# Kernel optimization log

Measured on AMD Instinct MI355X. Metric: run time of the kernel, lower is better.

## Reference

```python
import jax, jax.numpy as jnp
import numpy as np

B, N, M, C1, C2 = 16, 4096, 1024, 128, 256
MLP0, MLP1 = 256, 256
IN_CH = C1 + C2
EPS = 1e-5


def setup_inputs() -> dict:
    key = jax.random.key(0)
    ks = jax.random.split(key, 6)
    return {
        "xyz1": jax.random.normal(ks[0], (B, 3, N), jnp.float32),
        "xyz2": jax.random.normal(ks[1], (B, 3, M), jnp.float32),
        "points1": jax.random.normal(ks[2], (B, C1, N), jnp.float32),
        "points2": jax.random.normal(ks[3], (B, C2, M), jnp.float32),
        "W1": jax.random.normal(ks[4], (MLP0, IN_CH), jnp.float32) * (1.0 / np.sqrt(IN_CH)),
        "gamma1": jnp.ones((MLP0,), jnp.float32),
        "beta1": jnp.zeros((MLP0,), jnp.float32),
        "W2": jax.random.normal(ks[5], (MLP1, MLP0), jnp.float32) * (1.0 / np.sqrt(MLP0)),
        "gamma2": jnp.ones((MLP1,), jnp.float32),
        "beta2": jnp.zeros((MLP1,), jnp.float32),
    }


def _batchnorm(x, gamma, beta):
    # x: (B, N, C); normalize per channel over batch*length (training-mode BN, biased var)
    mean = jnp.mean(x, axis=(0, 1))
    var = jnp.mean((x - mean) ** 2, axis=(0, 1))
    return (x - mean) * jax.lax.rsqrt(var + EPS) * gamma + beta


def reference(xyz1, xyz2, points1, points2, W1, gamma1, beta1, W2, gamma2, beta2):
    p1 = jnp.swapaxes(xyz1, 1, 2)  # (B, N, 3)
    p2 = jnp.swapaxes(xyz2, 1, 2)  # (B, M, 3)
    # squared pairwise distances (B, N, M); squaring preserves 3-NN ordering,
    # and the original squares the euclidean dist before weighting anyway
    d2 = jnp.sum((p1[:, :, None, :] - p2[:, None, :, :]) ** 2, axis=-1)
    neg_d2, idx = jax.lax.top_k(-d2, 3)  # 3 smallest distances
    dist2 = jnp.maximum(-neg_d2, 1e-10)  # (B, N, 3)
    inv = 1.0 / dist2
    weight = inv / jnp.sum(inv, axis=-1, keepdims=True)  # (B, N, 3)
    f2 = jnp.swapaxes(points2, 1, 2)  # (B, M, C2)
    b, n, k = idx.shape
    gathered = jnp.take_along_axis(
        f2, idx.reshape(b, n * k)[:, :, None], axis=1
    ).reshape(b, n, k, -1)  # (B, N, 3, C2)
    interp = jnp.einsum("bnk,bnkc->bnc", weight, gathered)  # (B, N, C2)
    feat = jnp.concatenate([interp, jnp.swapaxes(points1, 1, 2)], axis=-1)  # (B, N, C1+C2)
    h = jnp.einsum("bnc,oc->bno", feat, W1)  # conv1d k=1, no bias
    h = jax.nn.relu(_batchnorm(h, gamma1, beta1))
    h = jnp.einsum("bnc,oc->bno", h, W2)
    h = jax.nn.relu(_batchnorm(h, gamma2, beta2))
    return jnp.swapaxes(h, 1, 2)  # (B, MLP1, N), channel-first like torch
```

## Files before the change

### kernel.cpp

```cpp
#include <hip/hip_runtime.h>

typedef unsigned short u16;
typedef unsigned int u32;

#define BB 16
#define NN 4096
#define MM 1024
#define C1V 128
#define C2V 256
#define O1 256
#define O2 256
#define EPSV 1e-5f
#define INV_CNT (1.0f/65536.0f)
#define NREP 32

typedef __attribute__((ext_vector_type(8))) short bf16x8;
typedef __attribute__((ext_vector_type(4))) float f32x4;

static __device__ __forceinline__ u16 f2b(float f) {
  u32 u = __float_as_uint(f);
  u32 r = (u + 0x7FFFu + ((u >> 16) & 1u)) >> 16;
  return (u16)r;
}
static __device__ __forceinline__ float b2f(u16 s) {
  return __uint_as_float(((u32)s) << 16);
}

#define GLD_LDS16(gp, lp)                                                      \
  __builtin_amdgcn_global_load_lds(                                            \
      (const __attribute__((address_space(1))) void*)(gp),                     \
      (__attribute__((address_space(3))) void*)(lp), 16, 0, 0)

__device__ __forceinline__ void tcast_tile(const float* __restrict__ in,
                                           u16* __restrict__ out, int C, int P,
                                           int p0, int c0, int b,
                                           float (*tile)[33]) {
  int tx = threadIdx.x & 31, ty = threadIdx.x >> 5;
  const float* ib = in + (size_t)b * C * P;
  u16* ob = out + (size_t)b * P * C;
#pragma unroll
  for (int i = 0; i < 4; ++i)
    tile[ty + i * 8][tx] = ib[(size_t)(c0 + ty + i * 8) * P + p0 + tx];
  __syncthreads();
#pragma unroll
  for (int i = 0; i < 4; ++i)
    ob[(size_t)(p0 + ty + i * 8) * C + c0 + tx] = f2b(tile[tx][ty + i * 8]);
}

__global__ __launch_bounds__(256) void prep_kernel(
    const float* __restrict__ xyz1, const float* __restrict__ xyz2,
    float* __restrict__ pd, int* __restrict__ pi,
    const float* __restrict__ points1, const float* __restrict__ points2,
    u16* __restrict__ p1t, u16* __restrict__ p2t,
    const float* __restrict__ W1, const float* __restrict__ W2,
    u16* __restrict__ W1b, u16* __restrict__ W2b,
    float* __restrict__ statsZero) {
  __shared__ float4 cand[256];
  __shared__ float tile[32][33];
  int bx = blockIdx.x;
  int t = threadIdx.x;

  if (bx < 512) {
    int c = bx & 3;
    int qt = (bx >> 2) & 7;
    int b = bx >> 5;
    const float* x2b = xyz2 + b * 3 * MM;
    {
      float x = x2b[c * 256 + t];
      float y = x2b[MM + c * 256 + t];
      float z = x2b[2 * MM + c * 256 + t];
      cand[t] = make_float4(x, y, z, x * x + y * y + z * z);
    }
    __syncthreads();
    const float* x1b = xyz1 + b * 3 * NN;
    int n0 = qt * 512 + t;
    int n1 = n0 + 256;
    float px0 = x1b[n0], py0 = x1b[NN + n0], pz0 = x1b[2 * NN + n0];
    float px1 = x1b[n1], py1 = x1b[NN + n1], pz1 = x1b[2 * NN + n1];
    const float INF = 3.4e38f;
    float k00 = INF, k01 = INF, k02 = INF;
    float k10 = INF, k11 = INF, k12 = INF;
    int j00 = 0, j01 = 0, j02 = 0;
    int j10 = 0, j11 = 0, j12 = 0;
#pragma unroll 8
    for (int m = 0; m < 256; ++m) {
      float4 cd = cand[m];
      {
        float dot = fmaf(px0, cd.x, fmaf(py0, cd.y, pz0 * cd.z));
        float key = fmaf(-2.0f, dot, cd.w);
        bool c0 = key < k00, c1 = key < k01, c2 = key < k02;
        k02 = c1 ? k01 : (c2 ? key : k02);
        j02 = c1 ? j01 : (c2 ? m : j02);
        k01 = c0 ? k00 : (c1 ? key : k01);
        j01 = c0 ? j00 : (c1 ? m : j01);
        k00 = c0 ? key : k00;
        j00 = c0 ? m : j00;
      }
      {
        float dot = fmaf(px1, cd.x, fmaf(py1, cd.y, pz1 * cd.z));
        float key = fmaf(-2.0f, dot, cd.w);
        bool c0 = key < k10, c1 = key < k11, c2 = key < k12;
        k12 = c1 ? k11 : (c2 ? key : k12);
        j12 = c1 ? j11 : (c2 ? m : j12);
        k11 = c0 ? k10 : (c1 ? key : k11);
        j11 = c0 ? j10 : (c1 ? m : j11);
        k10 = c0 ? key : k10;
        j10 = c0 ? m : j10;
      }
    }
    float pn0 = px0 * px0 + py0 * py0 + pz0 * pz0;
    float pn1 = px1 * px1 + py1 * py1 + pz1 * pz1;
    int gq0 = b * NN + n0;
    int gq1 = b * NN + n1;
    int base = c << 8;
    ((float4*)pd)[(size_t)c * 65536 + gq0] =
        make_float4(fmaxf(k00 + pn0, 1e-10f), fmaxf(k01 + pn0, 1e-10f),
                    fmaxf(k02 + pn0, 1e-10f), 0.0f);
    ((int4*)pi)[(size_t)c * 65536 + gq0] =
        make_int4(base + j00, base + j01, base + j02, 0);
    ((float4*)pd)[(size_t)c * 65536 + gq1] =
        make_float4(fmaxf(k10 + pn1, 1e-10f), fmaxf(k11 + pn1, 1e-10f),
                    fmaxf(k12 + pn1, 1e-10f), 0.0f);
    ((int4*)pi)[(size_t)c * 65536 + gq1] =
        make_int4(base + j10, base + j11, base + j12, 0);
  } else if (bx < 1152) {
    int i = (bx - 512) * 256 + t;
    if (i < 98304) W1b[i] = f2b(W1[i]);
    else if (i < 163840) W2b[i - 98304] = f2b(W2[i - 98304]);
  } else if (bx < 1184) {
    ((float4*)statsZero)[(bx - 1152) * 256 + t] =
        make_float4(0.f, 0.f, 0.f, 0.f);
  } else if (bx < 5280) {
    int local = bx - 1184;
    int pt = local & 31, ct = (local >> 5) & 7, b = local >> 8;
    tcast_tile(points2, p2t, C2V, MM, pt * 32, ct * 32, b, tile);
  } else {
    int local = bx - 5280;
    int pt = local & 127, ct = (local >> 7) & 3, b = local >> 9;
    tcast_tile(points1, p1t, C1V, NN, pt * 32, ct * 32, b, tile);
  }
}

template <int K, int NTILES, bool INTERP, bool STATS, bool OUTB, bool BNA>
__global__ __launch_bounds__(256) void gemm_mfma(
    const u16* __restrict__ A, int lda, const u16* __restrict__ B, int ldb,
    void* __restrict__ out, const u16* __restrict__ G,
    const float* __restrict__ pd, const int* __restrict__ pi,
    float* __restrict__ statsOut, const float* __restrict__ statsInR,
    const float* __restrict__ gamma, const float* __restrict__ beta) {
  __shared__ u16 smem[16384];
  __shared__ float wsh[128][3];
  __shared__ int ish[128][3];
  __shared__ float scA[256], shA[256];

  int t = threadIdx.x;
  int w = t >> 6, l = t & 63;
  int n0;
  if (NTILES > 0) {
    int p = blockIdx.x;
    int batch = ((p & 7) << 1) | ((p >> 3) & 1);
    int nt = p >> 4;
    n0 = (batch * NTILES + nt) * 128;
  } else {
    n0 = blockIdx.x * 128;
  }
  int o0 = blockIdx.y * 128;

  if (INTERP) {
    if (t < 128) {
      int gq = n0 + t;
      float4 d0 = ((const float4*)pd)[gq];
      int4 ii0 = ((const int4*)pi)[gq];
      float a0 = d0.x, a1 = d0.y, a2 = d0.z;
      int b0 = ii0.x, b1 = ii0.y, b2 = ii0.z;
#pragma unroll
      for (int c = 1; c < 4; ++c) {
        float4 dc = ((const float4*)pd)[(size_t)c * 65536 + gq];
        int4 ic = ((const int4*)pi)[(size_t)c * 65536 + gq];
        float kv[3] = {dc.x, dc.y, dc.z};
        int jv[3] = {ic.x, ic.y, ic.z};
#pragma unroll
        for (int j = 0; j < 3; ++j) {
          float key = kv[j];
          int idx = jv[j];
          bool c0 = key < a0, c1 = key < a1, c2 = key < a2;
          a2 = c1 ? a1 : (c2 ? key : a2);
          b2 = c1 ? b1 : (c2 ? idx : b2);
          a1 = c0 ? a0 : (c1 ? key : a1);
          b1 = c0 ? b0 : (c1 ? idx : b1);
          a0 = c0 ? key : a0;
          b0 = c0 ? idx : b0;
        }
      }
      float v0 = 1.0f / a0, v1 = 1.0f / a1, v2 = 1.0f / a2;
      float s = 1.0f / (v0 + v1 + v2);
      wsh[t][0] = v0 * s; wsh[t][1] = v1 * s; wsh[t][2] = v2 * s;
      ish[t][0] = b0;     ish[t][1] = b1;     ish[t][2] = b2;
    }
  }
  if (BNA) {
    float s = 0.0f, qq = 0.0f;
#pragma unroll
    for (int r = 0; r < NREP; ++r) {
      s += statsInR[r * 512 + t];
      qq += statsInR[r * 512 + 256 + t];
    }
    float mean = s * INV_CNT;
    float var = qq * INV_CNT - mean * mean;
    float sc = rsqrtf(var + EPSV) * gamma[t];
    scA[t] = sc;
    shA[t] = beta[t] - mean * sc;
  }

  int wm = w & 1, wn = w >> 1;
  int lr = l >> 2, lc = l & 3;
  int q = l >> 4, m = l & 15;

  f32x4 acc[4][4] = {};
  u16* As = smem;
  u16* Bs = smem + 4096;

  const u16* arow = A + (size_t)n0 * lda;
  const u16* brow = B + (size_t)o0 * ldb;

#pragma unroll
  for (int kt = 0; kt < K; kt += 32) {
    __syncthreads();
#pragma unroll
    for (int r = 0; r < 2; ++r) {
      int row = r * 64 + w * 16 + lr;
      if (BNA) {
        union { uint4 u; u16 s[8]; } v, o;
        v.u = *(const uint4*)(arow + (size_t)row * lda + kt + lc * 8);
        int cb = kt + lc * 8;
#pragma unroll
        for (int j = 0; j < 8; ++j) {
          float f = fmaf(b2f(v.s[j]), scA[cb + j], shA[cb + j]);
          o.s[j] = f2b(fmaxf(f, 0.0f));
        }
        *(uint4*)(As + row * 32 + lc * 8) = o.u;
      } else {
        GLD_LDS16(arow + (size_t)row * lda + kt + lc * 8, As + row * 32 + lc * 8);
      }
    }
#pragma unroll
    for (int r = 0; r < 2; ++r) {
      int row = r * 64 + w * 16 + lr;
      GLD_LDS16(brow + (size_t)row * ldb + kt + lc * 8, Bs + row * 32 + lc * 8);
    }
    __syncthreads();
    bf16x8 af[4], bf[4];
#pragma unroll
    for (int i = 0; i < 4; ++i)
      af[i] = *(const bf16x8*)(As + (wm * 64 + i * 16 + m) * 32 + q * 8);
#pragma unroll
    for (int j = 0; j < 4; ++j)
      bf[j] = *(const bf16x8*)(Bs + (wn * 64 + j * 16 + m) * 32 + q * 8);
#pragma unroll
    for (int i = 0; i < 4; ++i)
#pragma unroll
      for (int j = 0; j < 4; ++j)
        acc[i][j] =
            __builtin_amdgcn_mfma_f32_16x16x32_bf16(af[i], bf[j], acc[i][j], 0, 0, 0);
  }

  if (INTERP) {
    __syncthreads();
    int b = n0 >> 12;
    int rl = t >> 1, half = t & 1, rx = rl & 7;
    float w0 = wsh[rl][0], w1 = wsh[rl][1], w2 = wsh[rl][2];
    const u16* g0 = G + ((size_t)(b * 1024 + ish[rl][0])) * 256 + o0 + half * 64;
    const u16* g1 = G + ((size_t)(b * 1024 + ish[rl][1])) * 256 + o0 + half * 64;
    const u16* g2 = G + ((size_t)(b * 1024 + ish[rl][2])) * 256 + o0 + half * 64;
#pragma unroll
    for (int c8 = 0; c8 < 8; ++c8) {
      bf16x8 v0 = *(const bf16x8*)(g0 + c8 * 8);
      bf16x8 v1 = *(const bf16x8*)(g1 + c8 * 8);
      bf16x8 v2 = *(const bf16x8*)(g2 + c8 * 8);
      union { uint4 u; u16 s[8]; } o;
#pragma unroll
      for (int e = 0; e < 8; ++e) {
        float f = w0 * b2f((u16)v0[e]) + w1 * b2f((u16)v1[e]) +
                  w2 * b2f((u16)v2[e]);
        o.s[e] = f2b(f);
      }
      int ch = (half * 8 + c8) ^ rx;
      *(uint4*)(smem + rl * 128 + ch * 8) = o.u;
    }
    __syncthreads();
#pragma unroll
    for (int i = 0; i < 4; ++i)
#pragma unroll
      for (int reg = 0; reg < 4; ++reg) {
        int row = wm * 64 + i * 16 + q * 4 + reg;
        int rxr = row & 7;
#pragma unroll
        for (int j = 0; j < 4; ++j) {
          int col = wn * 64 + j * 16 + m;
          int off = row * 128 + (((col >> 3) ^ rxr) << 3) + (col & 7);
          acc[i][j][reg] += b2f(smem[off]);
        }
      }
  }

  if (STATS) {
    int rep = blockIdx.x & (NREP - 1);
#pragma unroll
    for (int j = 0; j < 4; ++j) {
      float s = 0.0f, ss = 0.0f;
#pragma unroll
      for (int i = 0; i < 4; ++i)
#pragma unroll
        for (int reg = 0; reg < 4; ++reg) {
          float v = acc[i][j][reg];
          s += v;
          ss += v * v;
        }
      s += __shfl_down(s, 32); ss += __shfl_down(ss, 32);
      s += __shfl_down(s, 16); ss += __shfl_down(ss, 16);
      if (l < 16) {
        int c = o0 + wn * 64 + j * 16 + l;
        atomicAdd(&statsOut[rep * 512 + c], s);
        atomicAdd(&statsOut[rep * 512 + 256 + c], ss);
      }
    }
  }

  if (OUTB) {
    __syncthreads();
#pragma unroll
    for (int i = 0; i < 4; ++i)
#pragma unroll
      for (int reg = 0; reg < 4; ++reg) {
        int row = wm * 64 + i * 16 + q * 4 + reg;
#pragma unroll
        for (int j = 0; j < 4; ++j)
          smem[row * 128 + wn * 64 + j * 16 + m] = f2b(acc[i][j][reg]);
      }
    __syncthreads();
    u16* outp = (u16*)out;
    int rbase = w * 32 + (l >> 4);
    int seg = l & 15;
#pragma unroll
    for (int itr = 0; itr < 8; ++itr) {
      int row = rbase + itr * 4;
      uint4 v = *(const uint4*)(smem + row * 128 + seg * 8);
      *(uint4*)(outp + (size_t)(n0 + row) * 256 + o0 + seg * 8) = v;
    }
  } else {
#pragma unroll
    for (int i = 0; i < 4; ++i) {
      int gr = n0 + wm * 64 + i * 16 + q * 4;
#pragma unroll
      for (int reg = 0; reg < 4; ++reg)
#pragma unroll
        for (int j = 0; j < 4; ++j) {
          int gc = o0 + wn * 64 + j * 16 + m;
          ((float*)out)[(size_t)(gr + reg) * 256 + gc] = acc[i][j][reg];
        }
    }
  }
}

__global__ __launch_bounds__(256) void bn2t_kernel(
    const u16* __restrict__ h2, const float* __restrict__ statsR,
    const float* __restrict__ gamma, const float* __restrict__ beta,
    float* __restrict__ out) {
  __shared__ float tile[32][33];
  __shared__ float sS[32], sH[32];
  int t = threadIdx.x;
  int tx = t & 31, ty = t >> 5;
  int n0 = blockIdx.x * 32, c0 = blockIdx.y * 32, b = blockIdx.z;
  if (t < 32) {
    int c = c0 + t;
    float s = 0.0f, qq = 0.0f;
#pragma unroll
    for (int r = 0; r < NREP; ++r) {
      s += statsR[r * 512 + c];
      qq += statsR[r * 512 + 256 + c];
    }
    float mean = s * INV_CNT;
    float var = qq * INV_CNT - mean * mean;
    float sc = rsqrtf(var + EPSV) * gamma[c];
    sS[t] = sc;
    sH[t] = beta[c] - mean * sc;
  }
  __syncthreads();
#pragma unroll
  for (int i = 0; i < 4; ++i) {
    int n = n0 + ty + i * 8;
    float v = b2f(h2[((size_t)b * NN + n) * 256 + c0 + tx]) * sS[tx] + sH[tx];
    tile[ty + i * 8][tx] = fmaxf(v, 0.0f);
  }
  __syncthreads();
#pragma unroll
  for (int i = 0; i < 4; ++i)
    out[((size_t)b * 256 + c0 + ty + i * 8) * NN + n0 + tx] = tile[tx][ty + i * 8];
}

extern "C" void kernel_launch(void* const* d_in, const int* in_sizes, int n_in,
                              void* d_out, int out_size, void* d_ws,
                              size_t ws_size, hipStream_t stream) {
  const float* xyz1    = (const float*)d_in[0];
  const float* xyz2    = (const float*)d_in[1];
  const float* points1 = (const float*)d_in[2];
  const float* points2 = (const float*)d_in[3];
  const float* W1      = (const float*)d_in[4];
  const float* gamma1  = (const float*)d_in[5];
  const float* beta1   = (const float*)d_in[6];
  const float* W2      = (const float*)d_in[7];
  const float* gamma2  = (const float*)d_in[8];
  const float* beta2   = (const float*)d_in[9];

  char* ws = (char*)d_ws;
  float* stats1R = (float*)(ws + 0);
  float* stats2R = (float*)(ws + 65536);
  u16*   W1b     = (u16*)(ws + 131072);
  u16*   W2b     = (u16*)(ws + 327680);
  u16*   p2t     = (u16*)(ws + 458752);
  u16*   p1t     = (u16*)(ws + 8847360);
  u16*   G       = (u16*)(ws + 25624576);
  u16*   h2b     = (u16*)(ws + 34013184);
  float* pd      = (float*)(ws + 67567616);
  int*   pi      = (int*)(ws + 71761920);
  u16*   h1b     = (u16*)d_out;
  float* out     = (float*)d_out;

  prep_kernel<<<13472, 256, 0, stream>>>(xyz1, xyz2, pd, pi, points1, points2,
                                         p1t, p2t, W1, W2, W1b, W2b, stats1R);
  gemm_mfma<256, 8, false, false, true, false><<<dim3(128, 2), 256, 0, stream>>>(
      p2t, 256, W1b, 384, G, nullptr, nullptr, nullptr, nullptr, nullptr,
      nullptr, nullptr);
  gemm_mfma<128, 32, true, true, true, false><<<dim3(512, 2), 256, 0, stream>>>(
      p1t, 128, W1b + 256, 384, h1b, G, pd, pi, stats1R, nullptr, nullptr,
      nullptr);
  gemm_mfma<256, 0, false, true, true, true><<<dim3(512, 2), 256, 0, stream>>>(
      h1b, 256, W2b, 256, h2b, nullptr, nullptr, nullptr, stats2R, stats1R,
      gamma1, beta1);
  bn2t_kernel<<<dim3(128, 8, 16), 256, 0, stream>>>(h2b, stats2R, gamma2,
                                                    beta2, out);
}
```

Measured before the change: 232.5 us.

## Fuse BN2+ReLU+transpose into second GEMM via grid-wide barrier

```diff
diff --git a/kernel.cpp b/kernel.cpp
--- a/kernel.cpp
+++ b/kernel.cpp
@@ -8,8 +8,6 @@
 #define MM 1024
 #define C1V 128
 #define C2V 256
-#define O1 256
-#define O2 256
 #define EPSV 1e-5f
 #define INV_CNT (1.0f/65536.0f)
 #define NREP 32
@@ -54,7 +52,7 @@
     u16* __restrict__ p1t, u16* __restrict__ p2t,
     const float* __restrict__ W1, const float* __restrict__ W2,
     u16* __restrict__ W1b, u16* __restrict__ W2b,
-    float* __restrict__ statsZero) {
+    float* __restrict__ statsZero, int* __restrict__ bar) {
   __shared__ float4 cand[256];
   __shared__ float tile[32][33];
   int bx = blockIdx.x;
@@ -130,6 +128,7 @@
   } else if (bx < 1184) {
     ((float4*)statsZero)[(bx - 1152) * 256 + t] =
         make_float4(0.f, 0.f, 0.f, 0.f);
+    if (bx == 1152 && t == 0) *bar = 0;
   } else if (bx < 5280) {
     int local = bx - 1184;
     int pt = local & 31, ct = (local >> 5) & 7, b = local >> 8;
@@ -141,17 +140,21 @@
   }
 }
 
-template <int K, int NTILES, bool INTERP, bool STATS, bool OUTB, bool BNA>
-__global__ __launch_bounds__(256) void gemm_mfma(
+template <int K, int NTILES, int NJ, bool INTERP, bool STATS, bool OUTB,
+          bool BNA, bool FUSE>
+__global__ __launch_bounds__(256, 2) void gemm_mfma(
     const u16* __restrict__ A, int lda, const u16* __restrict__ B, int ldb,
     void* __restrict__ out, const u16* __restrict__ G,
     const float* __restrict__ pd, const int* __restrict__ pi,
     float* __restrict__ statsOut, const float* __restrict__ statsInR,
-    const float* __restrict__ gamma, const float* __restrict__ beta) {
-  __shared__ u16 smem[16384];
+    const float* __restrict__ gamma, const float* __restrict__ beta,
+    const float* __restrict__ gamma2, const float* __restrict__ beta2,
+    int* bar, float* __restrict__ fout) {
+  __shared__ __align__(16) u16 smem[NJ == 8 ? 16896 : 16384];
   __shared__ float wsh[128][3];
   __shared__ int ish[128][3];
   __shared__ float scA[256], shA[256];
+  __shared__ float scB[256], shB[256];
 
   int t = threadIdx.x;
   int w = t >> 6, l = t & 63;
@@ -164,7 +167,7 @@
   } else {
     n0 = blockIdx.x * 128;
   }
-  int o0 = blockIdx.y * 128;
+  int o0 = blockIdx.y * (NJ * 32);
 
   if (INTERP) {
     if (t < 128) {
@@ -216,7 +219,7 @@
   int lr = l >> 2, lc = l & 3;
   int q = l >> 4, m = l & 15;
 
-  f32x4 acc[4][4] = {};
+  f32x4 acc[4][NJ] = {};
   u16* As = smem;
   u16* Bs = smem + 4096;
 
@@ -244,22 +247,22 @@
       }
     }
 #pragma unroll
-    for (int r = 0; r < 2; ++r) {
+    for (int r = 0; r < NJ / 2; ++r) {
       int row = r * 64 + w * 16 + lr;
       GLD_LDS16(brow + (size_t)row * ldb + kt + lc * 8, Bs + row * 32 + lc * 8);
     }
     __syncthreads();
-    bf16x8 af[4], bf[4];
+    bf16x8 af[4], bf[NJ];
 #pragma unroll
     for (int i = 0; i < 4; ++i)
       af[i] = *(const bf16x8*)(As + (wm * 64 + i * 16 + m) * 32 + q * 8);
 #pragma unroll
-    for (int j = 0; j < 4; ++j)
-      bf[j] = *(const bf16x8*)(Bs + (wn * 64 + j * 16 + m) * 32 + q * 8);
+    for (int j = 0; j < NJ; ++j)
+      bf[j] = *(const bf16x8*)(Bs + (wn * (NJ * 16) + j * 16 + m) * 32 + q * 8);
 #pragma unroll
     for (int i = 0; i < 4; ++i)
 #pragma unroll
-      for (int j = 0; j < 4; ++j)
+      for (int j = 0; j < NJ; ++j)
         acc[i][j] =
             __builtin_amdgcn_mfma_f32_16x16x32_bf16(af[i], bf[j], acc[i][j], 0, 0, 0);
   }
@@ -295,8 +298,8 @@
         int row = wm * 64 + i * 16 + q * 4 + reg;
         int rxr = row & 7;
 #pragma unroll
-        for (int j = 0; j < 4; ++j) {
-          int col = wn * 64 + j * 16 + m;
+        for (int j = 0; j < NJ; ++j) {
+          int col = wn * (NJ * 16) + j * 16 + m;
           int off = row * 128 + (((col >> 3) ^ rxr) << 3) + (col & 7);
           acc[i][j][reg] += b2f(smem[off]);
         }
@@ -306,7 +309,7 @@
   if (STATS) {
     int rep = blockIdx.x & (NREP - 1);
 #pragma unroll
-    for (int j = 0; j < 4; ++j) {
+    for (int j = 0; j < NJ; ++j) {
       float s = 0.0f, ss = 0.0f;
 #pragma unroll
       for (int i = 0; i < 4; ++i)
@@ -319,7 +322,7 @@
       s += __shfl_down(s, 32); ss += __shfl_down(ss, 32);
       s += __shfl_down(s, 16); ss += __shfl_down(ss, 16);
       if (l < 16) {
-        int c = o0 + wn * 64 + j * 16 + l;
+        int c = o0 + wn * (NJ * 16) + j * 16 + l;
         atomicAdd(&statsOut[rep * 512 + c], s);
         atomicAdd(&statsOut[rep * 512 + 256 + c], ss);
       }
@@ -334,8 +337,8 @@
       for (int reg = 0; reg < 4; ++reg) {
         int row = wm * 64 + i * 16 + q * 4 + reg;
 #pragma unroll
-        for (int j = 0; j < 4; ++j)
-          smem[row * 128 + wn * 64 + j * 16 + m] = f2b(acc[i][j][reg]);
+        for (int j = 0; j < NJ; ++j)
+          smem[row * 128 + wn * (NJ * 16) + j * 16 + m] = f2b(acc[i][j][reg]);
       }
     __syncthreads();
     u16* outp = (u16*)out;
@@ -347,6 +350,63 @@
       uint4 v = *(const uint4*)(smem + row * 128 + seg * 8);
       *(uint4*)(outp + (size_t)(n0 + row) * 256 + o0 + seg * 8) = v;
     }
+  } else if (FUSE) {
+    __syncthreads();
+    if (t == 0) {
+      __hip_atomic_fetch_add(bar, 1, __ATOMIC_ACQ_REL, __HIP_MEMORY_SCOPE_AGENT);
+      while (__hip_atomic_load(bar, __ATOMIC_ACQUIRE, __HIP_MEMORY_SCOPE_AGENT) <
+             (int)gridDim.x)
+        __builtin_amdgcn_s_sleep(8);
+    }
+    __syncthreads();
+    {
+      float s = 0.0f, qq = 0.0f;
+#pragma unroll
+      for (int r = 0; r < NREP; ++r) {
+        s += __hip_atomic_load(&statsOut[r * 512 + t], __ATOMIC_RELAXED,
+                               __HIP_MEMORY_SCOPE_AGENT);
+        qq += __hip_atomic_load(&statsOut[r * 512 + 256 + t], __ATOMIC_RELAXED,
+                                __HIP_MEMORY_SCOPE_AGENT);
+      }
+      float mean = s * INV_CNT;
+      float var = qq * INV_CNT - mean * mean;
+      float sc = rsqrtf(var + EPSV) * gamma2[t];
+      scB[t] = sc;
+      shB[t] = beta2[t] - mean * sc;
+    }
+    __syncthreads();
+    int b = n0 >> 12, nin = n0 & 4095;
+#pragma unroll
+    for (int h = 0; h < 2; ++h) {
+      if (h) __syncthreads();
+      if (wn == h) {
+#pragma unroll
+        for (int i = 0; i < 4; ++i)
+#pragma unroll
+          for (int j = 0; j < NJ; ++j) {
+            int c = j * 16 + m;
+            float sc = scB[h * 128 + c], sh = shB[h * 128 + c];
+#pragma unroll
+            for (int reg = 0; reg < 4; ++reg) {
+              int row = wm * 64 + i * 16 + q * 4 + reg;
+              smem[c * 132 + row] =
+                  f2b(fmaxf(fmaf(acc[i][j][reg], sc, sh), 0.0f));
+            }
+          }
+      }
+      __syncthreads();
+      int hl = l >> 5, nl = (l & 31) * 4;
+#pragma unroll
+      for (int it = 0; it < 16; ++it) {
+        int cl = w * 32 + it * 2 + hl;
+        uint2 vv = *(const uint2*)(smem + cl * 132 + nl);
+        float4 o4 = make_float4(
+            b2f((u16)(vv.x & 0xffff)), b2f((u16)(vv.x >> 16)),
+            b2f((u16)(vv.y & 0xffff)), b2f((u16)(vv.y >> 16)));
+        *(float4*)(fout + ((size_t)(b * 256 + h * 128 + cl)) * 4096 + nin + nl) =
+            o4;
+      }
+    }
   } else {
 #pragma unroll
     for (int i = 0; i < 4; ++i) {
@@ -354,48 +414,12 @@
 #pragma unroll
       for (int reg = 0; reg < 4; ++reg)
 #pragma unroll
-        for (int j = 0; j < 4; ++j) {
-          int gc = o0 + wn * 64 + j * 16 + m;
+        for (int j = 0; j < NJ; ++j) {
+          int gc = o0 + wn * (NJ * 16) + j * 16 + m;
           ((float*)out)[(size_t)(gr + reg) * 256 + gc] = acc[i][j][reg];
         }
     }
   }
-}
-
-__global__ __launch_bounds__(256) void bn2t_kernel(
-    const u16* __restrict__ h2, const float* __restrict__ statsR,
-    const float* __restrict__ gamma, const float* __restrict__ beta,
-    float* __restrict__ out) {
-  __shared__ float tile[32][33];
-  __shared__ float sS[32], sH[32];
-  int t = threadIdx.x;
-  int tx = t & 31, ty = t >> 5;
-  int n0 = blockIdx.x * 32, c0 = blockIdx.y * 32, b = blockIdx.z;
-  if (t < 32) {
-    int c = c0 + t;
-    float s = 0.0f, qq = 0.0f;
-#pragma unroll
-    for (int r = 0; r < NREP; ++r) {
-      s += statsR[r * 512 + c];
-      qq += statsR[r * 512 + 256 + c];
-    }
-    float mean = s * INV_CNT;
-    float var = qq * INV_CNT - mean * mean;
-    float sc = rsqrtf(var + EPSV) * gamma[c];
-    sS[t] = sc;
-    sH[t] = beta[c] - mean * sc;
-  }
-  __syncthreads();
-#pragma unroll
-  for (int i = 0; i < 4; ++i) {
-    int n = n0 + ty + i * 8;
-    float v = b2f(h2[((size_t)b * NN + n) * 256 + c0 + tx]) * sS[tx] + sH[tx];
-    tile[ty + i * 8][tx] = fmaxf(v, 0.0f);
-  }
-  __syncthreads();
-#pragma unroll
-  for (int i = 0; i < 4; ++i)
-    out[((size_t)b * 256 + c0 + ty + i * 8) * NN + n0 + tx] = tile[tx][ty + i * 8];
 }
 
 extern "C" void kernel_launch(void* const* d_in, const int* in_sizes, int n_in,
@@ -420,23 +444,25 @@
   u16*   p2t     = (u16*)(ws + 458752);
   u16*   p1t     = (u16*)(ws + 8847360);
   u16*   G       = (u16*)(ws + 25624576);
-  u16*   h2b     = (u16*)(ws + 34013184);
   float* pd      = (float*)(ws + 67567616);
   int*   pi      = (int*)(ws + 71761920);
+  int*   bar     = (int*)(ws + 75956224);
   u16*   h1b     = (u16*)d_out;
   float* out     = (float*)d_out;
 
   prep_kernel<<<13472, 256, 0, stream>>>(xyz1, xyz2, pd, pi, points1, points2,
-                                         p1t, p2t, W1, W2, W1b, W2b, stats1R);
-  gemm_mfma<256, 8, false, false, true, false><<<dim3(128, 2), 256, 0, stream>>>(
-      p2t, 256, W1b, 384, G, nullptr, nullptr, nullptr, nullptr, nullptr,
-      nullptr, nullptr);
-  gemm_mfma<128, 32, true, true, true, false><<<dim3(512, 2), 256, 0, stream>>>(
-      p1t, 128, W1b + 256, 384, h1b, G, pd, pi, stats1R, nullptr, nullptr,
-      nullptr);
-  gemm_mfma<256, 0, false, true, true, true><<<dim3(512, 2), 256, 0, stream>>>(
-      h1b, 256, W2b, 256, h2b, nullptr, nullptr, nullptr, stats2R, stats1R,
-      gamma1, beta1);
-  bn2t_kernel<<<dim3(128, 8, 16), 256, 0, stream>>>(h2b, stats2R, gamma2,
-                                                    beta2, out);
-}
+                                         p1t, p2t, W1, W2, W1b, W2b, stats1R,
+                                         bar);
+  gemm_mfma<256, 8, 4, false, false, true, false, false>
+      <<<dim3(128, 2), 256, 0, stream>>>(
+          p2t, 256, W1b, 384, G, nullptr, nullptr, nullptr, nullptr, nullptr,
+          nullptr, nullptr, nullptr, nullptr, nullptr, nullptr);
+  gemm_mfma<128, 32, 4, true, true, true, false, false>
+      <<<dim3(512, 2), 256, 0, stream>>>(
+          p1t, 128, W1b + 256, 384, h1b, G, pd, pi, stats1R, nullptr, nullptr,
+          nullptr, nullptr, nullptr, nullptr, nullptr);
+  gemm_mfma<256, 0, 8, false, true, false, true, true>
+      <<<dim3(512, 1), 256, 0, stream>>>(
+          h1b, 256, W2b, 256, nullptr, nullptr, nullptr, nullptr, stats2R,
+          stats1R, gamma1, beta1, gamma2, beta2, bar, out);
+}
```

After: 256.9 us. 10.5% more time.

## Replace second GEMM with 64-row full-width tile kernel fusing BN1+ReLU on A

Applied to the files above, without the earlier changes.

```diff
diff --git a/kernel.cpp b/kernel.cpp
--- a/kernel.cpp
+++ b/kernel.cpp
@@ -8,8 +8,6 @@
 #define MM 1024
 #define C1V 128
 #define C2V 256
-#define O1 256
-#define O2 256
 #define EPSV 1e-5f
 #define INV_CNT (1.0f/65536.0f)
 #define NREP 32
@@ -362,6 +360,118 @@
   }
 }
 
+__global__ __launch_bounds__(256) void gemm2_64(
+    const u16* __restrict__ A, const u16* __restrict__ B,
+    u16* __restrict__ out, float* __restrict__ statsOut,
+    const float* __restrict__ statsInR, const float* __restrict__ gamma,
+    const float* __restrict__ beta) {
+  __shared__ __align__(16) u16 smem[16384];
+  __shared__ float scA[256], shA[256];
+  int t = threadIdx.x;
+  int w = t >> 6, l = t & 63;
+  int n0 = blockIdx.x * 64;
+
+  {
+    float s = 0.0f, qq = 0.0f;
+#pragma unroll
+    for (int r = 0; r < NREP; ++r) {
+      s += statsInR[r * 512 + t];
+      qq += statsInR[r * 512 + 256 + t];
+    }
+    float mean = s * INV_CNT;
+    float var = qq * INV_CNT - mean * mean;
+    float sc = rsqrtf(var + EPSV) * gamma[t];
+    scA[t] = sc;
+    shA[t] = beta[t] - mean * sc;
+  }
+
+  int q = l >> 4, m = l & 15;
+  int sr = l >> 2, lc = l & 3;
+
+  f32x4 acc[4][4] = {};
+  u16* As = smem;
+  u16* Bs = smem + 2048;
+  const u16* arow = A + (size_t)n0 * 256;
+
+#pragma unroll
+  for (int kt = 0; kt < 256; kt += 32) {
+    __syncthreads();
+    {
+      int row = w * 16 + sr;
+      union { uint4 u; u16 s[8]; } v, o;
+      v.u = *(const uint4*)(arow + (size_t)row * 256 + kt + lc * 8);
+      int cb = kt + lc * 8;
+#pragma unroll
+      for (int j = 0; j < 8; ++j) {
+        float f = fmaf(b2f(v.s[j]), scA[cb + j], shA[cb + j]);
+        o.s[j] = f2b(fmaxf(f, 0.0f));
+      }
+      *(uint4*)(As + row * 32 + lc * 8) = o.u;
+    }
+#pragma unroll
+    for (int r = 0; r < 4; ++r) {
+      int row = r * 64 + w * 16 + sr;
+      GLD_LDS16(B + (size_t)row * 256 + kt + lc * 8, Bs + row * 32 + lc * 8);
+    }
+    __syncthreads();
+    bf16x8 af[4], bf[4];
+#pragma unroll
+    for (int i = 0; i < 4; ++i)
+      af[i] = *(const bf16x8*)(As + (i * 16 + m) * 32 + q * 8);
+#pragma unroll
+    for (int j = 0; j < 4; ++j)
+      bf[j] = *(const bf16x8*)(Bs + (w * 64 + j * 16 + m) * 32 + q * 8);
+#pragma unroll
+    for (int i = 0; i < 4; ++i)
+#pragma unroll
+      for (int j = 0; j < 4; ++j)
+        acc[i][j] =
+            __builtin_amdgcn_mfma_f32_16x16x32_bf16(af[i], bf[j], acc[i][j], 0, 0, 0);
+  }
+
+  {
+    int rep = blockIdx.x & (NREP - 1);
+#pragma unroll
+    for (int j = 0; j < 4; ++j) {
+      float s = 0.0f, ss = 0.0f;
+#pragma unroll
+      for (int i = 0; i < 4; ++i)
+#pragma unroll
+        for (int reg = 0; reg < 4; ++reg) {
+          float v = acc[i][j][reg];
+          s += v;
+          ss += v * v;
+        }
+      s += __shfl_down(s, 32); ss += __shfl_down(ss, 32);
+      s += __shfl_down(s, 16); ss += __shfl_down(ss, 16);
+      if (l < 16) {
+        int c = w * 64 + j * 16 + l;
+        atomicAdd(&statsOut[rep * 512 + c], s);
+        atomicAdd(&statsOut[rep * 512 + 256 + c], ss);
+      }
+    }
+  }
+
+  __syncthreads();
+#pragma unroll
+  for (int i = 0; i < 4; ++i)
+#pragma unroll
+    for (int reg = 0; reg < 4; ++reg) {
+      int row = i * 16 + q * 4 + reg;
+#pragma unroll
+      for (int j = 0; j < 4; ++j)
+        smem[row * 256 + w * 64 + j * 16 + m] = f2b(acc[i][j][reg]);
+    }
+  __syncthreads();
+  int rbase = t >> 5, seg = t & 31;
+#pragma unroll
+  for (int itr = 0; itr < 8; ++itr) {
+    int row = rbase + itr * 8;
+    uint4 v = *(const uint4*)(smem + row * 256 + seg * 8);
+    *(uint4*)(out + (size_t)(n0 + row) * 256 + seg * 8) = v;
+  }
+}
+
 __global__ __launch_bounds__(256) void bn2t_kernel(
     const u16* __restrict__ h2, const float* __restrict__ statsR,
     const float* __restrict__ gamma, const float* __restrict__ beta,
@@ -434,9 +544,8 @@
   gemm_mfma<128, 32, true, true, true, false><<<dim3(512, 2), 256, 0, stream>>>(
       p1t, 128, W1b + 256, 384, h1b, G, pd, pi, stats1R, nullptr, nullptr,
       nullptr);
-  gemm_mfma<256, 0, false, true, true, true><<<dim3(512, 2), 256, 0, stream>>>(
-      h1b, 256, W2b, 256, h2b, nullptr, nullptr, nullptr, stats2R, stats1R,
-      gamma1, beta1);
+  gemm2_64<<<1024, 256, 0, stream>>>(h1b, W2b, h2b, stats2R, stats1R, gamma1,
+                                     beta1);
   bn2t_kernel<<<dim3(128, 8, 16), 256, 0, stream>>>(h2b, stats2R, gamma2,
                                                     beta2, out);
 }
```

After: 227.8 us. 1.02x faster.
